# Kernel tuning notes

Measured on AMD Instinct MI355X. Metric: run time of the kernel, lower is better.

## Reference

```python
import jax, jax.numpy as jnp
import numpy as np

N_NODES = 50000
N_EDGES = 800000
D = 128            # input_dim == output_dim (no zero-padding branch in GatedGraphConv)
N_ETYPES = 4
N_STEPS = 8
B = 50
MAX_NODES = 1400
HID = 256


def setup_inputs() -> dict:
    key = jax.random.key(0)
    ks = jax.random.split(key, 10)
    # ragged graph sizes: alternating 600 / 1400 nodes, sums exactly to N_NODES
    counts = np.tile(np.array([600, 1400], dtype=np.int32), B // 2)
    s_d = 1.0 / np.sqrt(D)
    s_h = 1.0 / np.sqrt(HID)
    return {
        "node_features": jax.random.normal(ks[0], (N_NODES, D), jnp.float32),
        "edge_src": jax.random.randint(ks[1], (N_EDGES,), 0, N_NODES, dtype=jnp.int32),
        "edge_dst": jax.random.randint(ks[2], (N_EDGES,), 0, N_NODES, dtype=jnp.int32),
        "edge_types": jax.random.randint(ks[3], (N_EDGES,), 0, N_ETYPES, dtype=jnp.int32),
        "node_counts": jnp.asarray(counts),
        # per-edge-type message linears (DGL: one nn.Linear(out,out) per etype)
        "W_msg": jax.random.normal(ks[4], (N_ETYPES, D, D), jnp.float32) * s_d,
        "b_msg": jnp.zeros((N_ETYPES, D), jnp.float32),
        # GRUCell params (torch gate order: r, z, n)
        "W_ih": jax.random.normal(ks[5], (3 * D, D), jnp.float32) * s_d,
        "W_hh": jax.random.normal(ks[6], (3 * D, D), jnp.float32) * s_d,
        "b_ih": jnp.zeros((3 * D,), jnp.float32),
        "b_hh": jnp.zeros((3 * D,), jnp.float32),
        # classifier: Linear(D,256) + ReLU + Linear(256,1) + sigmoid (dropout = identity at eval)
        "W1": jax.random.normal(ks[7], (D, HID), jnp.float32) * s_d,
        "b1": jnp.zeros((HID,), jnp.float32),
        "W2": jax.random.normal(ks[8], (HID, 1), jnp.float32) * s_h,
        "b2": jnp.zeros((1,), jnp.float32),
    }


def _forward(node_features, edge_src, edge_dst, edge_types, node_counts,
             W_msg, b_msg, W_ih, W_hh, b_ih, b_hh, W1, b1, W2, b2):
    h = node_features
    for _ in range(N_STEPS):
        h_src = h[edge_src]                                   # [E, D] gather
        m = jnp.zeros_like(h_src)
        for t in range(N_ETYPES):                             # small fixed loop over edge types
            m = m + jnp.where((edge_types == t)[:, None],
                              h_src @ W_msg[t] + b_msg[t], 0.0)
        a = jax.ops.segment_sum(m, edge_dst, num_segments=N_NODES)  # [N, D] scatter-sum
        # GRUCell update
        gi = a @ W_ih.T + b_ih
        gh = h @ W_hh.T + b_hh
        i_r, i_z, i_n = jnp.split(gi, 3, axis=-1)
        h_r, h_z, h_n = jnp.split(gh, 3, axis=-1)
        r = jax.nn.sigmoid(i_r + h_r)
        z = jax.nn.sigmoid(i_z + h_z)
        n = jnp.tanh(i_n + r * h_n)
        h = (1.0 - z) * n + z * h
    # de-batchify to padded [B, MAX_NODES, D] + masked mean pool
    offsets = jnp.concatenate([jnp.zeros((1,), node_counts.dtype),
                               jnp.cumsum(node_counts)[:-1]])
    idx = offsets[:, None] + jnp.arange(MAX_NODES, dtype=node_counts.dtype)
    mask = jnp.arange(MAX_NODES)[None, :] < node_counts[:, None]
    g = h[jnp.clip(idx, 0, N_NODES - 1)] * mask[..., None]    # [B, MAX_NODES, D]
    pooled = g.sum(axis=1) / node_counts[:, None].astype(h.dtype)
    x = jax.nn.relu(pooled @ W1 + b1)
    return jax.nn.sigmoid(x @ W2 + b2)                        # [B, 1]


def reference(node_features, edge_src, edge_dst, edge_types, node_counts,
              W_msg, b_msg, W_ih, W_hh, b_ih, b_hh, W1, b1, W2, b2):
    return _forward(node_features, edge_src, edge_dst, edge_types, node_counts,
                    W_msg, b_msg, W_ih, W_hh, b_ih, b_hh, W1, b1, W2, b2)
```

## Files before the change

### kernel.cpp

```cpp
#include <hip/hip_runtime.h>
#include <hip/hip_bf16.h>

#define N_NODES 50000
#define N_EDGES 800000
#define D 128
#define N_ETYPES 4
#define N_STEPS 8
#define B_GRAPHS 50
#define HID 256
#define POOL_SPLIT 16
#define SCAN_B 196

typedef __attribute__((ext_vector_type(8))) short short8;
typedef __attribute__((ext_vector_type(4))) float f32x4;
typedef __attribute__((ext_vector_type(4))) unsigned uint4v;

static __device__ __forceinline__ unsigned short f2bf(float f) {
    union { float f; unsigned u; } v; v.f = f;
    unsigned r = v.u + 0x7FFF + ((v.u >> 16) & 1);
    return (unsigned short)(r >> 16);
}
static __device__ __forceinline__ float bf2f_u(unsigned s) {
    union { unsigned u; float f; } v; v.u = s << 16;
    return v.f;
}
static __device__ __forceinline__ float fsigmoid(float x) {
    return 1.f / (1.f + __expf(-x));
}
static __device__ __forceinline__ float ftanh(float x) {
    return 2.f / (1.f + __expf(-2.f * x)) - 1.f;
}

__global__ void k_init_h(const float* __restrict__ nf, unsigned short* __restrict__ hbf) {
    int i = blockIdx.x * blockDim.x + threadIdx.x;
    if (i < N_NODES * D) hbf[i] = f2bf(nf[i]);
}

__global__ void k_hist(const int* __restrict__ dst, int* __restrict__ deg) {
    int e = blockIdx.x * blockDim.x + threadIdx.x;
    if (e < N_EDGES) atomicAdd(&deg[dst[e]], 1);
}

__global__ __launch_bounds__(256) void k_scan1(const int* __restrict__ deg,
                                               int* __restrict__ bsum) {
    __shared__ int tmp[256];
    int t = threadIdx.x;
    int i = blockIdx.x * 256 + t;
    tmp[t] = (i < N_NODES) ? deg[i] : 0;
    __syncthreads();
    for (int s = 128; s > 0; s >>= 1) {
        if (t < s) tmp[t] += tmp[t + s];
        __syncthreads();
    }
    if (t == 0) bsum[blockIdx.x] = tmp[0];
}

__global__ __launch_bounds__(256) void k_scan2(const int* __restrict__ bsum,
                                               int* __restrict__ bpfx,
                                               int* __restrict__ rowptr) {
    __shared__ int part[256];
    int t = threadIdx.x;
    int v = (t < SCAN_B) ? bsum[t] : 0;
    part[t] = v;
    __syncthreads();
    for (int off = 1; off < 256; off <<= 1) {
        int u = (t >= off) ? part[t - off] : 0;
        __syncthreads();
        part[t] += u;
        __syncthreads();
    }
    if (t < SCAN_B) bpfx[t] = part[t] - v;
    if (t == SCAN_B - 1) rowptr[N_NODES] = part[t];
}

__global__ __launch_bounds__(256) void k_scan3(const int* __restrict__ deg,
                                               const int* __restrict__ bpfx,
                                               int* __restrict__ rowptr,
                                               int* __restrict__ cursor) {
    __shared__ int part[256];
    int t = threadIdx.x;
    int i = blockIdx.x * 256 + t;
    int v = (i < N_NODES) ? deg[i] : 0;
    part[t] = v;
    __syncthreads();
    for (int off = 1; off < 256; off <<= 1) {
        int u = (t >= off) ? part[t - off] : 0;
        __syncthreads();
        part[t] += u;
        __syncthreads();
    }
    if (i < N_NODES) {
        int rp = bpfx[blockIdx.x] + part[t] - v;
        rowptr[i] = rp;
        cursor[i] = rp;
    }
}

__global__ void k_fill(const int* __restrict__ src, const int* __restrict__ dst,
                       const int* __restrict__ et, int* __restrict__ cursor,
                       int* __restrict__ epack) {
    int e = blockIdx.x * blockDim.x + threadIdx.x;
    if (e < N_EDGES) {
        int slot = atomicAdd(&cursor[dst[e]], 1);
        epack[slot] = src[e] | (et[e] << 16);
    }
}

__global__ void k_pack(const float* __restrict__ Wmsg, const float* __restrict__ Wih,
                       const float* __restrict__ Whh, unsigned short* __restrict__ Pmsg,
                       unsigned short* __restrict__ Pih, unsigned short* __restrict__ Phh) {
    int bt = blockIdx.x;
    int l = threadIdx.x;
    if (bt < 128) {
        int nt = bt >> 4, kc = bt & 15;
        int n = nt * 16 + (l & 15);
        unsigned short* out = Pmsg + (((size_t)bt * 64 + l) * 8);
#pragma unroll
        for (int i = 0; i < 8; ++i) {
            int k = kc * 32 + ((l >> 4) << 3) + i;
            out[i] = f2bf(Wmsg[(size_t)(k >> 7) * (D * D) + (k & 127) * D + n]);
        }
        return;
    }
    const float* src;
    unsigned short* dstp;
    int id;
    if (bt < 224) { id = bt - 128; src = Wih; dstp = Pih; }
    else          { id = bt - 224; src = Whh; dstp = Phh; }
    int nt = id >> 2, c = id & 3;
    int n = nt * 16 + (l & 15);
    unsigned short* out = dstp + (((size_t)(nt * 4 + c) * 64 + l) * 8);
#pragma unroll
    for (int i = 0; i < 8; ++i) {
        int k = c * 32 + ((l >> 4) << 3) + i;
        out[i] = f2bf(src[n * D + k]);
    }
}

__global__ void k_pack_bias(const float* __restrict__ bih, const float* __restrict__ bhh,
                            float4* __restrict__ gb4) {
    int c = threadIdx.x;
    float4 g;
    g.x = bih[c] + bhh[c];
    g.y = bih[128 + c] + bhh[128 + c];
    g.z = bih[256 + c];
    g.w = bhh[256 + c];
    gb4[c] = g;
}

__global__ __launch_bounds__(256) void k_aggregate_s(const unsigned short* __restrict__ hbf,
                                                     const int* __restrict__ rowptr,
                                                     const int* __restrict__ epack,
                                                     unsigned short* __restrict__ S,
                                                     unsigned* __restrict__ deg4) {
    int w = threadIdx.x >> 6, l = threadIdx.x & 63;
    int v = blockIdx.x * 4 + w;
    if (v >= N_NODES) return;
    int lo = rowptr[v], hi = rowptr[v + 1];
    float a00 = 0.f, a01 = 0.f, a10 = 0.f, a11 = 0.f;
    float a20 = 0.f, a21 = 0.f, a30 = 0.f, a31 = 0.f;
    unsigned c0 = 0, c1 = 0, c2 = 0, c3 = 0;
    int i = lo;
    for (; i + 4 <= hi; i += 4) {
        int e0 = epack[i], e1 = epack[i + 1], e2 = epack[i + 2], e3 = epack[i + 3];
        unsigned x0 = *(const unsigned*)(hbf + ((size_t)(e0 & 0xFFFF) << 7) + 2 * l);
        unsigned x1 = *(const unsigned*)(hbf + ((size_t)(e1 & 0xFFFF) << 7) + 2 * l);
        unsigned x2 = *(const unsigned*)(hbf + ((size_t)(e2 & 0xFFFF) << 7) + 2 * l);
        unsigned x3 = *(const unsigned*)(hbf + ((size_t)(e3 & 0xFFFF) << 7) + 2 * l);
#define ACC_EDGE(e, x)                                                        \
        {                                                                     \
            int t_ = (e) >> 16;                                               \
            float lo_ = bf2f_u((x) & 0xFFFF), hi_ = bf2f_u((x) >> 16);        \
            if (t_ == 0)      { a00 += lo_; a01 += hi_; c0++; }               \
            else if (t_ == 1) { a10 += lo_; a11 += hi_; c1++; }               \
            else if (t_ == 2) { a20 += lo_; a21 += hi_; c2++; }               \
            else              { a30 += lo_; a31 += hi_; c3++; }               \
        }
        ACC_EDGE(e0, x0) ACC_EDGE(e1, x1) ACC_EDGE(e2, x2) ACC_EDGE(e3, x3)
    }
    for (; i < hi; ++i) {
        int e0 = epack[i];
        unsigned x0 = *(const unsigned*)(hbf + ((size_t)(e0 & 0xFFFF) << 7) + 2 * l);
        ACC_EDGE(e0, x0)
    }
#undef ACC_EDGE
    unsigned* Srow = (unsigned*)(S + (size_t)v * 512);
    Srow[l]       = (unsigned)f2bf(a00) | ((unsigned)f2bf(a01) << 16);
    Srow[64 + l]  = (unsigned)f2bf(a10) | ((unsigned)f2bf(a11) << 16);
    Srow[128 + l] = (unsigned)f2bf(a20) | ((unsigned)f2bf(a21) << 16);
    Srow[192 + l] = (unsigned)f2bf(a30) | ((unsigned)f2bf(a31) << 16);
    if (l == 0) {
        uint4v dg = {c0, c1, c2, c3};
        *(uint4v*)(deg4 + (size_t)v * 4) = dg;
    }
}

__global__ __launch_bounds__(256) void k_gemm_a(const unsigned short* __restrict__ S,
                                                const unsigned short* __restrict__ Pmsg,
                                                const unsigned* __restrict__ deg4,
                                                const float* __restrict__ bmsg,
                                                unsigned short* __restrict__ abf) {
    int tid = threadIdx.x, w = tid >> 6, l = tid & 63;
    int base = blockIdx.x * 64 + w * 16;
    int lr = l & 15, kb = l >> 4;
    int arow = base + lr; if (arow >= N_NODES) arow = N_NODES - 1;
    const short8* Sr = (const short8*)(S + (size_t)arow * 512);
    short8 af[16];
#pragma unroll
    for (int kc = 0; kc < 16; ++kc) af[kc] = Sr[kc * 4 + kb];
    uint4v dg[4];
#pragma unroll
    for (int j = 0; j < 4; ++j) {
        int row = base + kb * 4 + j; if (row >= N_NODES) row = N_NODES - 1;
        dg[j] = *(const uint4v*)(deg4 + (size_t)row * 4);
    }
    const short8* Bp = (const short8*)Pmsg;
#pragma unroll
    for (int ntp = 0; ntp < 4; ++ntp) {
        f32x4 acc0 = {0.f, 0.f, 0.f, 0.f}, acc1 = {0.f, 0.f, 0.f, 0.f};
#pragma unroll
        for (int kc = 0; kc < 16; ++kc) {
            short8 b0 = Bp[(((ntp * 2 + 0) * 16 + kc) * 64) + l];
            short8 b1 = Bp[(((ntp * 2 + 1) * 16 + kc) * 64) + l];
            acc0 = __builtin_amdgcn_mfma_f32_16x16x32_bf16(af[kc], b0, acc0, 0, 0, 0);
            acc1 = __builtin_amdgcn_mfma_f32_16x16x32_bf16(af[kc], b1, acc1, 0, 0, 0);
        }
#pragma unroll
        for (int half = 0; half < 2; ++half) {
            f32x4 acc = half ? acc1 : acc0;
            int col = (ntp * 2 + half) * 16 + lr;
            float b0 = bmsg[col], b1 = bmsg[128 + col], b2 = bmsg[256 + col], b3 = bmsg[384 + col];
#pragma unroll
            for (int j = 0; j < 4; ++j) {
                int row = base + kb * 4 + j;
                if (row < N_NODES) {
                    float bias = (float)dg[j].x * b0 + (float)dg[j].y * b1 +
                                 (float)dg[j].z * b2 + (float)dg[j].w * b3;
                    abf[(size_t)row * D + col] = f2bf(acc[j] + bias);
                }
            }
        }
    }
}

__global__ __launch_bounds__(256) void k_gru(const unsigned short* __restrict__ abf,
                                             unsigned short* __restrict__ hbf,
                                             const unsigned short* __restrict__ Pih,
                                             const unsigned short* __restrict__ Phh,
                                             const float4* __restrict__ gb4) {
    int tid = threadIdx.x, w = tid >> 6, l = tid & 63;
    int base = (blockIdx.x >> 1) * 64 + w * 16;
    int nt0 = (blockIdx.x & 1) * 4;
    int lr = l & 15, kb = l >> 4;
    int arow = base + lr; if (arow >= N_NODES) arow = N_NODES - 1;
    const short8* ar = (const short8*)(abf + (size_t)arow * D);
    const short8* hr = (const short8*)(hbf + (size_t)arow * D);
    short8 afa[4], afh[4];
#pragma unroll
    for (int c = 0; c < 4; ++c) { afa[c] = ar[c * 4 + kb]; afh[c] = hr[c * 4 + kb]; }
    const short8* Bi = (const short8*)Pih;
    const short8* Bh = (const short8*)Phh;
#pragma unroll
    for (int ntl = 0; ntl < 4; ++ntl) {
        int nt = nt0 + ntl;
        f32x4 racc = {0.f, 0.f, 0.f, 0.f};
        f32x4 zacc = {0.f, 0.f, 0.f, 0.f};
        f32x4 giacc = {0.f, 0.f, 0.f, 0.f};
        f32x4 ghacc = {0.f, 0.f, 0.f, 0.f};
#pragma unroll
        for (int c = 0; c < 4; ++c) {
            short8 bir = Bi[((0 * 8 + nt) * 4 + c) * 64 + l];
            short8 bhr = Bh[((0 * 8 + nt) * 4 + c) * 64 + l];
            short8 biz = Bi[((1 * 8 + nt) * 4 + c) * 64 + l];
            short8 bhz = Bh[((1 * 8 + nt) * 4 + c) * 64 + l];
            short8 bin = Bi[((2 * 8 + nt) * 4 + c) * 64 + l];
            short8 bhn = Bh[((2 * 8 + nt) * 4 + c) * 64 + l];
            racc = __builtin_amdgcn_mfma_f32_16x16x32_bf16(afa[c], bir, racc, 0, 0, 0);
            racc = __builtin_amdgcn_mfma_f32_16x16x32_bf16(afh[c], bhr, racc, 0, 0, 0);
            zacc = __builtin_amdgcn_mfma_f32_16x16x32_bf16(afa[c], biz, zacc, 0, 0, 0);
            zacc = __builtin_amdgcn_mfma_f32_16x16x32_bf16(afh[c], bhz, zacc, 0, 0, 0);
            giacc = __builtin_amdgcn_mfma_f32_16x16x32_bf16(afa[c], bin, giacc, 0, 0, 0);
            ghacc = __builtin_amdgcn_mfma_f32_16x16x32_bf16(afh[c], bhn, ghacc, 0, 0, 0);
        }
        int col = nt * 16 + lr;
        float4 gb = gb4[col];
#pragma unroll
        for (int j = 0; j < 4; ++j) {
            int row = base + kb * 4 + j;
            if (row < N_NODES) {
                float rr = fsigmoid(racc[j] + gb.x);
                float zz = fsigmoid(zacc[j] + gb.y);
                float nn = ftanh(giacc[j] + gb.z + rr * (ghacc[j] + gb.w));
                size_t idx = (size_t)row * D + col;
                float hold = bf2f_u(hbf[idx]);
                hbf[idx] = f2bf((1.f - zz) * nn + zz * hold);
            }
        }
    }
}

__global__ __launch_bounds__(256) void k_pool1(const unsigned short* __restrict__ hbf,
                                               const int* __restrict__ counts,
                                               float* __restrict__ partial) {
    __shared__ float tmp[256];
    int g = blockIdx.x / POOL_SPLIT;
    int j = blockIdx.x % POOL_SPLIT;
    int t = threadIdx.x;
    int offset = 0;
    for (int i = 0; i < g; ++i) offset += counts[i];
    int cnt = counts[g];
    int d = t & 127, half = t >> 7;
    float acc = 0.f;
    for (int r = 2 * j + half; r < cnt; r += 2 * POOL_SPLIT)
        acc += bf2f_u(hbf[(size_t)(offset + r) * D + d]);
    tmp[t] = acc;
    __syncthreads();
    if (t < D) partial[(size_t)(g * POOL_SPLIT + j) * D + t] = tmp[t] + tmp[t + 128];
}

__global__ __launch_bounds__(256) void k_pool2(const float* __restrict__ partial,
                                               const int* __restrict__ counts,
                                               const float* __restrict__ W1,
                                               const float* __restrict__ b1,
                                               const float* __restrict__ W2,
                                               const float* __restrict__ b2,
                                               float* __restrict__ out) {
    __shared__ float pooled[D];
    __shared__ float xh[HID];
    int g = blockIdx.x;
    int t = threadIdx.x;
    int cnt = counts[g];
    if (t < D) {
        float s = 0.f;
#pragma unroll
        for (int j = 0; j < POOL_SPLIT; ++j)
            s += partial[(size_t)(g * POOL_SPLIT + j) * D + t];
        pooled[t] = s / (float)cnt;
    }
    __syncthreads();
    float x = b1[t];
    for (int k = 0; k < D; ++k) x += pooled[k] * W1[k * HID + t];
    x = fmaxf(x, 0.f);
    xh[t] = x * W2[t];
    __syncthreads();
    for (int s = 128; s > 0; s >>= 1) {
        if (t < s) xh[t] += xh[t + s];
        __syncthreads();
    }
    if (t == 0) out[g] = 1.f / (1.f + __expf(-(xh[0] + b2[0])));
}

extern "C" void kernel_launch(void* const* d_in, const int* in_sizes, int n_in,
                              void* d_out, int out_size, void* d_ws, size_t ws_size,
                              hipStream_t stream) {
    const float* nf   = (const float*)d_in[0];
    const int* esrc   = (const int*)d_in[1];
    const int* edst   = (const int*)d_in[2];
    const int* etyp   = (const int*)d_in[3];
    const int* counts = (const int*)d_in[4];
    const float* Wmsg = (const float*)d_in[5];
    const float* bmsg = (const float*)d_in[6];
    const float* Wih  = (const float*)d_in[7];
    const float* Whh  = (const float*)d_in[8];
    const float* bih  = (const float*)d_in[9];
    const float* bhh  = (const float*)d_in[10];
    const float* W1   = (const float*)d_in[11];
    const float* b1   = (const float*)d_in[12];
    const float* W2   = (const float*)d_in[13];
    const float* b2   = (const float*)d_in[14];
    float* out = (float*)d_out;

    char* ws = (char*)d_ws;
    size_t off = 0;
    auto alloc = [&](size_t bytes) {
        void* p = ws + off;
        off = (off + bytes + 255) & ~(size_t)255;
        return p;
    };
    unsigned short* hbf = (unsigned short*)alloc((size_t)N_NODES * D * 2);
    unsigned short* abf = (unsigned short*)alloc((size_t)N_NODES * D * 2);
    unsigned short* S   = (unsigned short*)alloc((size_t)N_NODES * 512 * 2);
    unsigned short* Pmsg = (unsigned short*)alloc(128 * 64 * 8 * 2);
    unsigned short* Pih  = (unsigned short*)alloc(24 * 4 * 64 * 8 * 2);
    unsigned short* Phh  = (unsigned short*)alloc(24 * 4 * 64 * 8 * 2);
    float* gb4 = (float*)alloc(128 * 16);
    int* deg    = (int*)alloc((size_t)N_NODES * 4);
    unsigned* deg4 = (unsigned*)alloc((size_t)N_NODES * 16);
    int* rowptr = (int*)alloc((size_t)(N_NODES + 1) * 4);
    int* cursor = (int*)alloc((size_t)N_NODES * 4);
    int* epack  = (int*)alloc((size_t)N_EDGES * 4);
    float* partial = (float*)alloc((size_t)B_GRAPHS * POOL_SPLIT * D * 4);
    int* bsum = (int*)alloc(SCAN_B * 4);
    int* bpfx = (int*)alloc(SCAN_B * 4);

    hipMemsetAsync(deg, 0, (size_t)N_NODES * 4, stream);
    k_init_h<<<(N_NODES * D) / 256, 256, 0, stream>>>(nf, hbf);
    k_hist<<<N_EDGES / 256, 256, 0, stream>>>(edst, deg);
    k_scan1<<<SCAN_B, 256, 0, stream>>>(deg, bsum);
    k_scan2<<<1, 256, 0, stream>>>(bsum, bpfx, rowptr);
    k_scan3<<<SCAN_B, 256, 0, stream>>>(deg, bpfx, rowptr, cursor);
    k_fill<<<N_EDGES / 256, 256, 0, stream>>>(esrc, edst, etyp, cursor, epack);
    k_pack<<<320, 64, 0, stream>>>(Wmsg, Wih, Whh, Pmsg, Pih, Phh);
    k_pack_bias<<<1, 128, 0, stream>>>(bih, bhh, (float4*)gb4);

    int ga_blocks  = (N_NODES + 63) / 64;
    int gru_blocks = 2 * ((N_NODES + 63) / 64);
    int agg_blocks = (N_NODES + 3) / 4;
    for (int s = 0; s < N_STEPS; ++s) {
        k_aggregate_s<<<agg_blocks, 256, 0, stream>>>(hbf, rowptr, epack, S, deg4);
        k_gemm_a<<<ga_blocks, 256, 0, stream>>>(S, Pmsg, deg4, bmsg, abf);
        k_gru<<<gru_blocks, 256, 0, stream>>>(abf, hbf, Pih, Phh, (const float4*)gb4);
    }
    k_pool1<<<B_GRAPHS * POOL_SPLIT, 256, 0, stream>>>(hbf, counts, partial);
    k_pool2<<<B_GRAPHS, 256, 0, stream>>>(partial, counts, W1, b1, W2, b2, out);
}
```

Baseline: 1.065 ms.

## Fuse aggregation, message GEMM and GRU into one per-step kernel

Replaces the three per-step kernels (aggregate, message GEMM, GRU) with a single kernel. Each block handles 16 nodes and keeps the per-type sums and messages in swizzled shared memory instead of global S/abf buffers, with ping-pong h buffers so the in-place update stays race-free. This removes the global round-trips for S (1 KB per node) and abf, plus two launches per step. In exchange blocks are smaller (16 rows), each block re-reads all weight fragments, and the GEMM phases may run at lower occupancy because of the larger shared-memory footprint.

```diff
diff --git a/kernel.cpp b/kernel.cpp
--- a/kernel.cpp
+++ b/kernel.cpp
@@ -10,6 +10,7 @@
 #define HID 256
 #define POOL_SPLIT 16
 #define SCAN_B 196
+#define NPB 16
 
 typedef __attribute__((ext_vector_type(8))) short short8;
 typedef __attribute__((ext_vector_type(4))) float f32x4;
@@ -19,6 +20,9 @@
     union { float f; unsigned u; } v; v.f = f;
     unsigned r = v.u + 0x7FFF + ((v.u >> 16) & 1);
     return (unsigned short)(r >> 16);
+}
+static __device__ __forceinline__ unsigned pk2(float a, float b) {
+    return (unsigned)f2bf(a) | ((unsigned)f2bf(b) << 16);
 }
 static __device__ __forceinline__ float bf2f_u(unsigned s) {
     union { unsigned u; float f; } v; v.u = s << 16;
@@ -148,152 +152,146 @@
     gb4[c] = g;
 }
 
-__global__ __launch_bounds__(256) void k_aggregate_s(const unsigned short* __restrict__ hbf,
-                                                     const int* __restrict__ rowptr,
-                                                     const int* __restrict__ epack,
-                                                     unsigned short* __restrict__ S,
-                                                     unsigned* __restrict__ deg4) {
-    int w = threadIdx.x >> 6, l = threadIdx.x & 63;
-    int v = blockIdx.x * 4 + w;
-    if (v >= N_NODES) return;
-    int lo = rowptr[v], hi = rowptr[v + 1];
-    float a00 = 0.f, a01 = 0.f, a10 = 0.f, a11 = 0.f;
-    float a20 = 0.f, a21 = 0.f, a30 = 0.f, a31 = 0.f;
-    unsigned c0 = 0, c1 = 0, c2 = 0, c3 = 0;
-    int i = lo;
-    for (; i + 4 <= hi; i += 4) {
-        int e0 = epack[i], e1 = epack[i + 1], e2 = epack[i + 2], e3 = epack[i + 3];
-        unsigned x0 = *(const unsigned*)(hbf + ((size_t)(e0 & 0xFFFF) << 7) + 2 * l);
-        unsigned x1 = *(const unsigned*)(hbf + ((size_t)(e1 & 0xFFFF) << 7) + 2 * l);
-        unsigned x2 = *(const unsigned*)(hbf + ((size_t)(e2 & 0xFFFF) << 7) + 2 * l);
-        unsigned x3 = *(const unsigned*)(hbf + ((size_t)(e3 & 0xFFFF) << 7) + 2 * l);
+__global__ __launch_bounds__(256) void k_step(const unsigned short* __restrict__ hold,
+                                              unsigned short* __restrict__ hnew,
+                                              const int* __restrict__ rowptr,
+                                              const int* __restrict__ epack,
+                                              const unsigned short* __restrict__ Pmsg,
+                                              const unsigned short* __restrict__ Pih,
+                                              const unsigned short* __restrict__ Phh,
+                                              const float* __restrict__ bmsg,
+                                              const float4* __restrict__ gb4) {
+    __shared__ unsigned short Sh[NPB * 512];
+    __shared__ unsigned short Ah[NPB * 128];
+    __shared__ uint4v Dg[NPB];
+    int tid = threadIdx.x, w = tid >> 6, l = tid & 63;
+    int lr = l & 15, kb = l >> 4;
+    int nb = blockIdx.x * NPB;
+
+    for (int q = 0; q < 4; ++q) {
+        int n = w * 4 + q;
+        int v = nb + n;
+        int lo = rowptr[v], hi = rowptr[v + 1];
+        float a00 = 0.f, a01 = 0.f, a10 = 0.f, a11 = 0.f;
+        float a20 = 0.f, a21 = 0.f, a30 = 0.f, a31 = 0.f;
+        unsigned c0 = 0, c1 = 0, c2 = 0, c3 = 0;
+        int i = lo;
+        for (; i + 4 <= hi; i += 4) {
+            int e0 = epack[i], e1 = epack[i + 1], e2 = epack[i + 2], e3 = epack[i + 3];
+            unsigned x0 = *(const unsigned*)(hold + ((size_t)(e0 & 0xFFFF) << 7) + 2 * l);
+            unsigned x1 = *(const unsigned*)(hold + ((size_t)(e1 & 0xFFFF) << 7) + 2 * l);
+            unsigned x2 = *(const unsigned*)(hold + ((size_t)(e2 & 0xFFFF) << 7) + 2 * l);
+            unsigned x3 = *(const unsigned*)(hold + ((size_t)(e3 & 0xFFFF) << 7) + 2 * l);
 #define ACC_EDGE(e, x)                                                        \
-        {                                                                     \
-            int t_ = (e) >> 16;                                               \
-            float lo_ = bf2f_u((x) & 0xFFFF), hi_ = bf2f_u((x) >> 16);        \
-            if (t_ == 0)      { a00 += lo_; a01 += hi_; c0++; }               \
-            else if (t_ == 1) { a10 += lo_; a11 += hi_; c1++; }               \
-            else if (t_ == 2) { a20 += lo_; a21 += hi_; c2++; }               \
-            else              { a30 += lo_; a31 += hi_; c3++; }               \
-        }
-        ACC_EDGE(e0, x0) ACC_EDGE(e1, x1) ACC_EDGE(e2, x2) ACC_EDGE(e3, x3)
-    }
-    for (; i < hi; ++i) {
-        int e0 = epack[i];
-        unsigned x0 = *(const unsigned*)(hbf + ((size_t)(e0 & 0xFFFF) << 7) + 2 * l);
-        ACC_EDGE(e0, x0)
-    }
+            {                                                                 \
+                int t_ = (e) >> 16;                                           \
+                float lo_ = bf2f_u((x) & 0xFFFF), hi_ = bf2f_u((x) >> 16);    \
+                if (t_ == 0)      { a00 += lo_; a01 += hi_; c0++; }           \
+                else if (t_ == 1) { a10 += lo_; a11 += hi_; c1++; }           \
+                else if (t_ == 2) { a20 += lo_; a21 += hi_; c2++; }           \
+                else              { a30 += lo_; a31 += hi_; c3++; }           \
+            }
+            ACC_EDGE(e0, x0) ACC_EDGE(e1, x1) ACC_EDGE(e2, x2) ACC_EDGE(e3, x3)
+        }
+        for (; i < hi; ++i) {
+            int e0 = epack[i];
+            unsigned x0 = *(const unsigned*)(hold + ((size_t)(e0 & 0xFFFF) << 7) + 2 * l);
+            ACC_EDGE(e0, x0)
+        }
 #undef ACC_EDGE
-    unsigned* Srow = (unsigned*)(S + (size_t)v * 512);
-    Srow[l]       = (unsigned)f2bf(a00) | ((unsigned)f2bf(a01) << 16);
-    Srow[64 + l]  = (unsigned)f2bf(a10) | ((unsigned)f2bf(a11) << 16);
-    Srow[128 + l] = (unsigned)f2bf(a20) | ((unsigned)f2bf(a21) << 16);
-    Srow[192 + l] = (unsigned)f2bf(a30) | ((unsigned)f2bf(a31) << 16);
-    if (l == 0) {
-        uint4v dg = {c0, c1, c2, c3};
-        *(uint4v*)(deg4 + (size_t)v * 4) = dg;
-    }
-}
-
-__global__ __launch_bounds__(256) void k_gemm_a(const unsigned short* __restrict__ S,
-                                                const unsigned short* __restrict__ Pmsg,
-                                                const unsigned* __restrict__ deg4,
-                                                const float* __restrict__ bmsg,
-                                                unsigned short* __restrict__ abf) {
-    int tid = threadIdx.x, w = tid >> 6, l = tid & 63;
-    int base = blockIdx.x * 64 + w * 16;
-    int lr = l & 15, kb = l >> 4;
-    int arow = base + lr; if (arow >= N_NODES) arow = N_NODES - 1;
-    const short8* Sr = (const short8*)(S + (size_t)arow * 512);
-    short8 af[16];
-#pragma unroll
-    for (int kc = 0; kc < 16; ++kc) af[kc] = Sr[kc * 4 + kb];
-    uint4v dg[4];
-#pragma unroll
-    for (int j = 0; j < 4; ++j) {
-        int row = base + kb * 4 + j; if (row >= N_NODES) row = N_NODES - 1;
-        dg[j] = *(const uint4v*)(deg4 + (size_t)row * 4);
-    }
-    const short8* Bp = (const short8*)Pmsg;
-#pragma unroll
-    for (int ntp = 0; ntp < 4; ++ntp) {
+        unsigned swz = (unsigned)((n & 7) << 4);
+        char* rowp = (char*)Sh + n * 1024;
+        *(unsigned*)(rowp + ((4 * l) ^ swz))        = pk2(a00, a01);
+        *(unsigned*)(rowp + ((256 + 4 * l) ^ swz))  = pk2(a10, a11);
+        *(unsigned*)(rowp + ((512 + 4 * l) ^ swz))  = pk2(a20, a21);
+        *(unsigned*)(rowp + ((768 + 4 * l) ^ swz))  = pk2(a30, a31);
+        if (l == 0) { uint4v dgv = {c0, c1, c2, c3}; Dg[n] = dgv; }
+    }
+    __syncthreads();
+
+    {
         f32x4 acc0 = {0.f, 0.f, 0.f, 0.f}, acc1 = {0.f, 0.f, 0.f, 0.f};
+        const short8* Bp = (const short8*)Pmsg;
+        unsigned rswz = (unsigned)((lr & 7) << 4);
 #pragma unroll
         for (int kc = 0; kc < 16; ++kc) {
-            short8 b0 = Bp[(((ntp * 2 + 0) * 16 + kc) * 64) + l];
-            short8 b1 = Bp[(((ntp * 2 + 1) * 16 + kc) * 64) + l];
-            acc0 = __builtin_amdgcn_mfma_f32_16x16x32_bf16(af[kc], b0, acc0, 0, 0, 0);
-            acc1 = __builtin_amdgcn_mfma_f32_16x16x32_bf16(af[kc], b1, acc1, 0, 0, 0);
-        }
-#pragma unroll
-        for (int half = 0; half < 2; ++half) {
-            f32x4 acc = half ? acc1 : acc0;
-            int col = (ntp * 2 + half) * 16 + lr;
+            short8 af = *(const short8*)((const char*)Sh + lr * 1024 +
+                                         (((unsigned)(kc * 64 + kb * 16)) ^ rswz));
+            short8 b0 = Bp[(size_t)(w * 16 + kc) * 64 + l];
+            short8 b1 = Bp[(size_t)((w + 4) * 16 + kc) * 64 + l];
+            acc0 = __builtin_amdgcn_mfma_f32_16x16x32_bf16(af, b0, acc0, 0, 0, 0);
+            acc1 = __builtin_amdgcn_mfma_f32_16x16x32_bf16(af, b1, acc1, 0, 0, 0);
+        }
+#pragma unroll
+        for (int t = 0; t < 2; ++t) {
+            int nt = w + t * 4;
+            int col = nt * 16 + lr;
             float b0 = bmsg[col], b1 = bmsg[128 + col], b2 = bmsg[256 + col], b3 = bmsg[384 + col];
+            f32x4 acc = t ? acc1 : acc0;
 #pragma unroll
             for (int j = 0; j < 4; ++j) {
-                int row = base + kb * 4 + j;
-                if (row < N_NODES) {
-                    float bias = (float)dg[j].x * b0 + (float)dg[j].y * b1 +
-                                 (float)dg[j].z * b2 + (float)dg[j].w * b3;
-                    abf[(size_t)row * D + col] = f2bf(acc[j] + bias);
-                }
+                int row = kb * 4 + j;
+                uint4v dgv = Dg[row];
+                float av = acc[j] + (float)dgv.x * b0 + (float)dgv.y * b1 +
+                           (float)dgv.z * b2 + (float)dgv.w * b3;
+                *(unsigned short*)((char*)Ah + row * 256 +
+                                   (((unsigned)(2 * col)) ^ ((unsigned)((row & 7) << 4)))) = f2bf(av);
             }
         }
     }
-}
-
-__global__ __launch_bounds__(256) void k_gru(const unsigned short* __restrict__ abf,
-                                             unsigned short* __restrict__ hbf,
-                                             const unsigned short* __restrict__ Pih,
-                                             const unsigned short* __restrict__ Phh,
-                                             const float4* __restrict__ gb4) {
-    int tid = threadIdx.x, w = tid >> 6, l = tid & 63;
-    int base = (blockIdx.x >> 1) * 64 + w * 16;
-    int nt0 = (blockIdx.x & 1) * 4;
-    int lr = l & 15, kb = l >> 4;
-    int arow = base + lr; if (arow >= N_NODES) arow = N_NODES - 1;
-    const short8* ar = (const short8*)(abf + (size_t)arow * D);
-    const short8* hr = (const short8*)(hbf + (size_t)arow * D);
-    short8 afa[4], afh[4];
-#pragma unroll
-    for (int c = 0; c < 4; ++c) { afa[c] = ar[c * 4 + kb]; afh[c] = hr[c * 4 + kb]; }
-    const short8* Bi = (const short8*)Pih;
-    const short8* Bh = (const short8*)Phh;
-#pragma unroll
-    for (int ntl = 0; ntl < 4; ++ntl) {
-        int nt = nt0 + ntl;
-        f32x4 racc = {0.f, 0.f, 0.f, 0.f};
-        f32x4 zacc = {0.f, 0.f, 0.f, 0.f};
-        f32x4 giacc = {0.f, 0.f, 0.f, 0.f};
-        f32x4 ghacc = {0.f, 0.f, 0.f, 0.f};
+    __syncthreads();
+
+    {
+        const short8* hrow = (const short8*)(hold + (size_t)(nb + lr) * D);
+        short8 afh[4];
+#pragma unroll
+        for (int c = 0; c < 4; ++c) afh[c] = hrow[c * 4 + kb];
+        f32x4 racc[2], zacc[2], giacc[2], ghacc[2];
+#pragma unroll
+        for (int t = 0; t < 2; ++t) {
+            racc[t] = (f32x4){0.f, 0.f, 0.f, 0.f};
+            zacc[t] = (f32x4){0.f, 0.f, 0.f, 0.f};
+            giacc[t] = (f32x4){0.f, 0.f, 0.f, 0.f};
+            ghacc[t] = (f32x4){0.f, 0.f, 0.f, 0.f};
+        }
+        const short8* Bi = (const short8*)Pih;
+        const short8* Bh = (const short8*)Phh;
+        unsigned rswz = (unsigned)((lr & 7) << 4);
 #pragma unroll
         for (int c = 0; c < 4; ++c) {
-            short8 bir = Bi[((0 * 8 + nt) * 4 + c) * 64 + l];
-            short8 bhr = Bh[((0 * 8 + nt) * 4 + c) * 64 + l];
-            short8 biz = Bi[((1 * 8 + nt) * 4 + c) * 64 + l];
-            short8 bhz = Bh[((1 * 8 + nt) * 4 + c) * 64 + l];
-            short8 bin = Bi[((2 * 8 + nt) * 4 + c) * 64 + l];
-            short8 bhn = Bh[((2 * 8 + nt) * 4 + c) * 64 + l];
-            racc = __builtin_amdgcn_mfma_f32_16x16x32_bf16(afa[c], bir, racc, 0, 0, 0);
-            racc = __builtin_amdgcn_mfma_f32_16x16x32_bf16(afh[c], bhr, racc, 0, 0, 0);
-            zacc = __builtin_amdgcn_mfma_f32_16x16x32_bf16(afa[c], biz, zacc, 0, 0, 0);
-            zacc = __builtin_amdgcn_mfma_f32_16x16x32_bf16(afh[c], bhz, zacc, 0, 0, 0);
-            giacc = __builtin_amdgcn_mfma_f32_16x16x32_bf16(afa[c], bin, giacc, 0, 0, 0);
-            ghacc = __builtin_amdgcn_mfma_f32_16x16x32_bf16(afh[c], bhn, ghacc, 0, 0, 0);
-        }
-        int col = nt * 16 + lr;
-        float4 gb = gb4[col];
-#pragma unroll
-        for (int j = 0; j < 4; ++j) {
-            int row = base + kb * 4 + j;
-            if (row < N_NODES) {
-                float rr = fsigmoid(racc[j] + gb.x);
-                float zz = fsigmoid(zacc[j] + gb.y);
-                float nn = ftanh(giacc[j] + gb.z + rr * (ghacc[j] + gb.w));
+            short8 afa = *(const short8*)((const char*)Ah + lr * 256 +
+                                          (((unsigned)(c * 64 + kb * 16)) ^ rswz));
+#pragma unroll
+            for (int t = 0; t < 2; ++t) {
+                int nt = w + t * 4;
+                short8 bir = Bi[(size_t)((0 + nt) * 4 + c) * 64 + l];
+                short8 bhr = Bh[(size_t)((0 + nt) * 4 + c) * 64 + l];
+                short8 biz = Bi[(size_t)((8 + nt) * 4 + c) * 64 + l];
+                short8 bhz = Bh[(size_t)((8 + nt) * 4 + c) * 64 + l];
+                short8 bin = Bi[(size_t)((16 + nt) * 4 + c) * 64 + l];
+                short8 bhn = Bh[(size_t)((16 + nt) * 4 + c) * 64 + l];
+                racc[t] = __builtin_amdgcn_mfma_f32_16x16x32_bf16(afa, bir, racc[t], 0, 0, 0);
+                racc[t] = __builtin_amdgcn_mfma_f32_16x16x32_bf16(afh[c], bhr, racc[t], 0, 0, 0);
+                zacc[t] = __builtin_amdgcn_mfma_f32_16x16x32_bf16(afa, biz, zacc[t], 0, 0, 0);
+                zacc[t] = __builtin_amdgcn_mfma_f32_16x16x32_bf16(afh[c], bhz, zacc[t], 0, 0, 0);
+                giacc[t] = __builtin_amdgcn_mfma_f32_16x16x32_bf16(afa, bin, giacc[t], 0, 0, 0);
+                ghacc[t] = __builtin_amdgcn_mfma_f32_16x16x32_bf16(afh[c], bhn, ghacc[t], 0, 0, 0);
+            }
+        }
+#pragma unroll
+        for (int t = 0; t < 2; ++t) {
+            int nt = w + t * 4;
+            int col = nt * 16 + lr;
+            float4 gb = gb4[col];
+#pragma unroll
+            for (int j = 0; j < 4; ++j) {
+                int row = nb + kb * 4 + j;
+                float rr = fsigmoid(racc[t][j] + gb.x);
+                float zz = fsigmoid(zacc[t][j] + gb.y);
+                float nn = ftanh(giacc[t][j] + gb.z + rr * (ghacc[t][j] + gb.w));
                 size_t idx = (size_t)row * D + col;
-                float hold = bf2f_u(hbf[idx]);
-                hbf[idx] = f2bf((1.f - zz) * nn + zz * hold);
+                float hv = bf2f_u(hold[idx]);
+                hnew[idx] = f2bf((1.f - zz) * nn + zz * hv);
             }
         }
     }
@@ -377,15 +375,13 @@
         off = (off + bytes + 255) & ~(size_t)255;
         return p;
     };
-    unsigned short* hbf = (unsigned short*)alloc((size_t)N_NODES * D * 2);
-    unsigned short* abf = (unsigned short*)alloc((size_t)N_NODES * D * 2);
-    unsigned short* S   = (unsigned short*)alloc((size_t)N_NODES * 512 * 2);
+    unsigned short* hbf0 = (unsigned short*)alloc((size_t)N_NODES * D * 2);
+    unsigned short* hbf1 = (unsigned short*)alloc((size_t)N_NODES * D * 2);
     unsigned short* Pmsg = (unsigned short*)alloc(128 * 64 * 8 * 2);
     unsigned short* Pih  = (unsigned short*)alloc(24 * 4 * 64 * 8 * 2);
     unsigned short* Phh  = (unsigned short*)alloc(24 * 4 * 64 * 8 * 2);
     float* gb4 = (float*)alloc(128 * 16);
     int* deg    = (int*)alloc((size_t)N_NODES * 4);
-    unsigned* deg4 = (unsigned*)alloc((size_t)N_NODES * 16);
     int* rowptr = (int*)alloc((size_t)(N_NODES + 1) * 4);
     int* cursor = (int*)alloc((size_t)N_NODES * 4);
     int* epack  = (int*)alloc((size_t)N_EDGES * 4);
@@ -394,7 +390,7 @@
     int* bpfx = (int*)alloc(SCAN_B * 4);
 
     hipMemsetAsync(deg, 0, (size_t)N_NODES * 4, stream);
-    k_init_h<<<(N_NODES * D) / 256, 256, 0, stream>>>(nf, hbf);
+    k_init_h<<<(N_NODES * D) / 256, 256, 0, stream>>>(nf, hbf0);
     k_hist<<<N_EDGES / 256, 256, 0, stream>>>(edst, deg);
     k_scan1<<<SCAN_B, 256, 0, stream>>>(deg, bsum);
     k_scan2<<<1, 256, 0, stream>>>(bsum, bpfx, rowptr);
@@ -403,14 +399,14 @@
     k_pack<<<320, 64, 0, stream>>>(Wmsg, Wih, Whh, Pmsg, Pih, Phh);
     k_pack_bias<<<1, 128, 0, stream>>>(bih, bhh, (float4*)gb4);
 
-    int ga_blocks  = (N_NODES + 63) / 64;
-    int gru_blocks = 2 * ((N_NODES + 63) / 64);
-    int agg_blocks = (N_NODES + 3) / 4;
+    const int step_blocks = N_NODES / NPB;
     for (int s = 0; s < N_STEPS; ++s) {
-        k_aggregate_s<<<agg_blocks, 256, 0, stream>>>(hbf, rowptr, epack, S, deg4);
-        k_gemm_a<<<ga_blocks, 256, 0, stream>>>(S, Pmsg, deg4, bmsg, abf);
-        k_gru<<<gru_blocks, 256, 0, stream>>>(abf, hbf, Pih, Phh, (const float4*)gb4);
-    }
-    k_pool1<<<B_GRAPHS * POOL_SPLIT, 256, 0, stream>>>(hbf, counts, partial);
+        const unsigned short* hold = (s & 1) ? hbf1 : hbf0;
+        unsigned short* hnew       = (s & 1) ? hbf0 : hbf1;
+        k_step<<<step_blocks, 256, 0, stream>>>(hold, hnew, rowptr, epack,
+                                                Pmsg, Pih, Phh, bmsg,
+                                                (const float4*)gb4);
+    }
+    k_pool1<<<B_GRAPHS * POOL_SPLIT, 256, 0, stream>>>(hbf0, counts, partial);
     k_pool2<<<B_GRAPHS, 256, 0, stream>>>(partial, counts, W1, b1, W2, b2, out);
 }
```

New measurement: 1.113 ms. 4.5% more time.

## Bucket CSR by (node, edge type) to remove per-edge type branching

Applied to the files above, without the earlier changes.

Builds the CSR keyed by node*4+etype, so each node's edges are pre-sorted by type. The aggregate kernel can then sum each type segment with branch-free code, using pre-shifted byte offsets, and derive degrees from rowptr instead of writing deg4. The message GEMM is split across twice as many blocks, and h is double-buffered between steps. This costs a larger scan over 200k entries and extra rowptr reads, and the inner loops for short per-type segments become shorter.

```diff
diff --git a/kernel.cpp b/kernel.cpp
--- a/kernel.cpp
+++ b/kernel.cpp
@@ -9,21 +9,34 @@
 #define B_GRAPHS 50
 #define HID 256
 #define POOL_SPLIT 16
-#define SCAN_B 196
+#define N4 (N_NODES * N_ETYPES)
+#define SCAN_B4 ((N4 + 255) / 256)
 
 typedef __attribute__((ext_vector_type(8))) short short8;
 typedef __attribute__((ext_vector_type(4))) float f32x4;
 typedef __attribute__((ext_vector_type(4))) unsigned uint4v;
+typedef __attribute__((ext_vector_type(4))) int int4v;
 
 static __device__ __forceinline__ unsigned short f2bf(float f) {
     union { float f; unsigned u; } v; v.f = f;
     unsigned r = v.u + 0x7FFF + ((v.u >> 16) & 1);
     return (unsigned short)(r >> 16);
 }
+static __device__ __forceinline__ unsigned pk2(float a, float b) {
+    return (unsigned)f2bf(a) | ((unsigned)f2bf(b) << 16);
+}
 static __device__ __forceinline__ float bf2f_u(unsigned s) {
     union { unsigned u; float f; } v; v.u = s << 16;
     return v.f;
 }
+static __device__ __forceinline__ float bflo(unsigned x) {
+    union { unsigned u; float f; } v; v.u = x << 16;
+    return v.f;
+}
+static __device__ __forceinline__ float bfhi(unsigned x) {
+    union { unsigned u; float f; } v; v.u = x & 0xFFFF0000u;
+    return v.f;
+}
 static __device__ __forceinline__ float fsigmoid(float x) {
     return 1.f / (1.f + __expf(-x));
 }
@@ -36,17 +49,18 @@
     if (i < N_NODES * D) hbf[i] = f2bf(nf[i]);
 }
 
-__global__ void k_hist(const int* __restrict__ dst, int* __restrict__ deg) {
+__global__ void k_hist(const int* __restrict__ dst, const int* __restrict__ et,
+                       int* __restrict__ deg4) {
     int e = blockIdx.x * blockDim.x + threadIdx.x;
-    if (e < N_EDGES) atomicAdd(&deg[dst[e]], 1);
-}
-
-__global__ __launch_bounds__(256) void k_scan1(const int* __restrict__ deg,
+    if (e < N_EDGES) atomicAdd(&deg4[dst[e] * 4 + et[e]], 1);
+}
+
+__global__ __launch_bounds__(256) void k_scan1(const int* __restrict__ deg4,
                                                int* __restrict__ bsum) {
     __shared__ int tmp[256];
     int t = threadIdx.x;
     int i = blockIdx.x * 256 + t;
-    tmp[t] = (i < N_NODES) ? deg[i] : 0;
+    tmp[t] = (i < N4) ? deg4[i] : 0;
     __syncthreads();
     for (int s = 128; s > 0; s >>= 1) {
         if (t < s) tmp[t] += tmp[t + s];
@@ -55,32 +69,32 @@
     if (t == 0) bsum[blockIdx.x] = tmp[0];
 }
 
-__global__ __launch_bounds__(256) void k_scan2(const int* __restrict__ bsum,
-                                               int* __restrict__ bpfx,
-                                               int* __restrict__ rowptr) {
-    __shared__ int part[256];
+__global__ __launch_bounds__(1024) void k_scan2(const int* __restrict__ bsum,
+                                                int* __restrict__ bpfx,
+                                                int* __restrict__ rowptr4) {
+    __shared__ int part[1024];
     int t = threadIdx.x;
-    int v = (t < SCAN_B) ? bsum[t] : 0;
+    int v = (t < SCAN_B4) ? bsum[t] : 0;
     part[t] = v;
     __syncthreads();
-    for (int off = 1; off < 256; off <<= 1) {
+    for (int off = 1; off < 1024; off <<= 1) {
         int u = (t >= off) ? part[t - off] : 0;
         __syncthreads();
         part[t] += u;
         __syncthreads();
     }
-    if (t < SCAN_B) bpfx[t] = part[t] - v;
-    if (t == SCAN_B - 1) rowptr[N_NODES] = part[t];
-}
-
-__global__ __launch_bounds__(256) void k_scan3(const int* __restrict__ deg,
+    if (t < SCAN_B4) bpfx[t] = part[t] - v;
+    if (t == SCAN_B4 - 1) rowptr4[N4] = part[t];
+}
+
+__global__ __launch_bounds__(256) void k_scan3(const int* __restrict__ deg4,
                                                const int* __restrict__ bpfx,
-                                               int* __restrict__ rowptr,
-                                               int* __restrict__ cursor) {
+                                               int* __restrict__ rowptr4,
+                                               int* __restrict__ cursor4) {
     __shared__ int part[256];
     int t = threadIdx.x;
     int i = blockIdx.x * 256 + t;
-    int v = (i < N_NODES) ? deg[i] : 0;
+    int v = (i < N4) ? deg4[i] : 0;
     part[t] = v;
     __syncthreads();
     for (int off = 1; off < 256; off <<= 1) {
@@ -89,20 +103,20 @@
         part[t] += u;
         __syncthreads();
     }
-    if (i < N_NODES) {
+    if (i < N4) {
         int rp = bpfx[blockIdx.x] + part[t] - v;
-        rowptr[i] = rp;
-        cursor[i] = rp;
+        rowptr4[i] = rp;
+        cursor4[i] = rp;
     }
 }
 
 __global__ void k_fill(const int* __restrict__ src, const int* __restrict__ dst,
-                       const int* __restrict__ et, int* __restrict__ cursor,
+                       const int* __restrict__ et, int* __restrict__ cursor4,
                        int* __restrict__ epack) {
     int e = blockIdx.x * blockDim.x + threadIdx.x;
     if (e < N_EDGES) {
-        int slot = atomicAdd(&cursor[dst[e]], 1);
-        epack[slot] = src[e] | (et[e] << 16);
+        int slot = atomicAdd(&cursor4[dst[e] * 4 + et[e]], 1);
+        epack[slot] = src[e] << 8;
     }
 }
 
@@ -148,94 +162,95 @@
     gb4[c] = g;
 }
 
-__global__ __launch_bounds__(256) void k_aggregate_s(const unsigned short* __restrict__ hbf,
-                                                     const int* __restrict__ rowptr,
+__global__ __launch_bounds__(256) void k_aggregate_s(const unsigned short* __restrict__ hold,
+                                                     const int* __restrict__ rowptr4,
                                                      const int* __restrict__ epack,
-                                                     unsigned short* __restrict__ S,
-                                                     unsigned* __restrict__ deg4) {
+                                                     unsigned short* __restrict__ S) {
     int w = threadIdx.x >> 6, l = threadIdx.x & 63;
     int v = blockIdx.x * 4 + w;
     if (v >= N_NODES) return;
-    int lo = rowptr[v], hi = rowptr[v + 1];
-    float a00 = 0.f, a01 = 0.f, a10 = 0.f, a11 = 0.f;
-    float a20 = 0.f, a21 = 0.f, a30 = 0.f, a31 = 0.f;
-    unsigned c0 = 0, c1 = 0, c2 = 0, c3 = 0;
-    int i = lo;
-    for (; i + 4 <= hi; i += 4) {
-        int e0 = epack[i], e1 = epack[i + 1], e2 = epack[i + 2], e3 = epack[i + 3];
-        unsigned x0 = *(const unsigned*)(hbf + ((size_t)(e0 & 0xFFFF) << 7) + 2 * l);
-        unsigned x1 = *(const unsigned*)(hbf + ((size_t)(e1 & 0xFFFF) << 7) + 2 * l);
-        unsigned x2 = *(const unsigned*)(hbf + ((size_t)(e2 & 0xFFFF) << 7) + 2 * l);
-        unsigned x3 = *(const unsigned*)(hbf + ((size_t)(e3 & 0xFFFF) << 7) + 2 * l);
-#define ACC_EDGE(e, x)                                                        \
-        {                                                                     \
-            int t_ = (e) >> 16;                                               \
-            float lo_ = bf2f_u((x) & 0xFFFF), hi_ = bf2f_u((x) >> 16);        \
-            if (t_ == 0)      { a00 += lo_; a01 += hi_; c0++; }               \
-            else if (t_ == 1) { a10 += lo_; a11 += hi_; c1++; }               \
-            else if (t_ == 2) { a20 += lo_; a21 += hi_; c2++; }               \
-            else              { a30 += lo_; a31 += hi_; c3++; }               \
-        }
-        ACC_EDGE(e0, x0) ACC_EDGE(e1, x1) ACC_EDGE(e2, x2) ACC_EDGE(e3, x3)
-    }
-    for (; i < hi; ++i) {
-        int e0 = epack[i];
-        unsigned x0 = *(const unsigned*)(hbf + ((size_t)(e0 & 0xFFFF) << 7) + 2 * l);
-        ACC_EDGE(e0, x0)
-    }
-#undef ACC_EDGE
+    int4v b = *(const int4v*)(rowptr4 + v * 4);
+    int b4 = rowptr4[v * 4 + 4];
+    const char* hp = (const char*)hold + 4 * l;
     unsigned* Srow = (unsigned*)(S + (size_t)v * 512);
-    Srow[l]       = (unsigned)f2bf(a00) | ((unsigned)f2bf(a01) << 16);
-    Srow[64 + l]  = (unsigned)f2bf(a10) | ((unsigned)f2bf(a11) << 16);
-    Srow[128 + l] = (unsigned)f2bf(a20) | ((unsigned)f2bf(a21) << 16);
-    Srow[192 + l] = (unsigned)f2bf(a30) | ((unsigned)f2bf(a31) << 16);
-    if (l == 0) {
-        uint4v dg = {c0, c1, c2, c3};
-        *(uint4v*)(deg4 + (size_t)v * 4) = dg;
+#pragma unroll
+    for (int t = 0; t < 4; ++t) {
+        int i  = (t == 0) ? b.x : (t == 1) ? b.y : (t == 2) ? b.z : b.w;
+        int hi = (t == 0) ? b.y : (t == 1) ? b.z : (t == 2) ? b.w : b4;
+        float a0 = 0.f, a1 = 0.f;
+        for (; i + 4 <= hi; i += 4) {
+            int s0 = epack[i], s1 = epack[i + 1], s2 = epack[i + 2], s3 = epack[i + 3];
+            unsigned x0 = *(const unsigned*)(hp + s0);
+            unsigned x1 = *(const unsigned*)(hp + s1);
+            unsigned x2 = *(const unsigned*)(hp + s2);
+            unsigned x3 = *(const unsigned*)(hp + s3);
+            a0 += bflo(x0) + bflo(x1) + bflo(x2) + bflo(x3);
+            a1 += bfhi(x0) + bfhi(x1) + bfhi(x2) + bfhi(x3);
+        }
+        if (i + 2 <= hi) {
+            int s0 = epack[i], s1 = epack[i + 1];
+            unsigned x0 = *(const unsigned*)(hp + s0);
+            unsigned x1 = *(const unsigned*)(hp + s1);
+            a0 += bflo(x0) + bflo(x1);
+            a1 += bfhi(x0) + bfhi(x1);
+            i += 2;
+        }
+        if (i < hi) {
+            unsigned x0 = *(const unsigned*)(hp + epack[i]);
+            a0 += bflo(x0);
+            a1 += bfhi(x0);
+        }
+        Srow[t * 64 + l] = pk2(a0, a1);
     }
 }
 
 __global__ __launch_bounds__(256) void k_gemm_a(const unsigned short* __restrict__ S,
                                                 const unsigned short* __restrict__ Pmsg,
-                                                const unsigned* __restrict__ deg4,
+                                                const int* __restrict__ rowptr4,
                                                 const float* __restrict__ bmsg,
                                                 unsigned short* __restrict__ abf) {
     int tid = threadIdx.x, w = tid >> 6, l = tid & 63;
-    int base = blockIdx.x * 64 + w * 16;
+    int base = (blockIdx.x >> 1) * 64 + w * 16;
+    int nh = (blockIdx.x & 1) * 4;
     int lr = l & 15, kb = l >> 4;
     int arow = base + lr; if (arow >= N_NODES) arow = N_NODES - 1;
     const short8* Sr = (const short8*)(S + (size_t)arow * 512);
     short8 af[16];
 #pragma unroll
     for (int kc = 0; kc < 16; ++kc) af[kc] = Sr[kc * 4 + kb];
-    uint4v dg[4];
+    float dgf[4][4];
 #pragma unroll
     for (int j = 0; j < 4; ++j) {
         int row = base + kb * 4 + j; if (row >= N_NODES) row = N_NODES - 1;
-        dg[j] = *(const uint4v*)(deg4 + (size_t)row * 4);
+        int4v r4 = *(const int4v*)(rowptr4 + row * 4);
+        int r5 = rowptr4[row * 4 + 4];
+        dgf[j][0] = (float)(r4.y - r4.x);
+        dgf[j][1] = (float)(r4.z - r4.y);
+        dgf[j][2] = (float)(r4.w - r4.z);
+        dgf[j][3] = (float)(r5 - r4.w);
     }
     const short8* Bp = (const short8*)Pmsg;
 #pragma unroll
-    for (int ntp = 0; ntp < 4; ++ntp) {
+    for (int ntp = 0; ntp < 2; ++ntp) {
+        int nt0 = nh + ntp * 2;
         f32x4 acc0 = {0.f, 0.f, 0.f, 0.f}, acc1 = {0.f, 0.f, 0.f, 0.f};
 #pragma unroll
         for (int kc = 0; kc < 16; ++kc) {
-            short8 b0 = Bp[(((ntp * 2 + 0) * 16 + kc) * 64) + l];
-            short8 b1 = Bp[(((ntp * 2 + 1) * 16 + kc) * 64) + l];
+            short8 b0 = Bp[(size_t)((nt0 + 0) * 16 + kc) * 64 + l];
+            short8 b1 = Bp[(size_t)((nt0 + 1) * 16 + kc) * 64 + l];
             acc0 = __builtin_amdgcn_mfma_f32_16x16x32_bf16(af[kc], b0, acc0, 0, 0, 0);
             acc1 = __builtin_amdgcn_mfma_f32_16x16x32_bf16(af[kc], b1, acc1, 0, 0, 0);
         }
 #pragma unroll
         for (int half = 0; half < 2; ++half) {
             f32x4 acc = half ? acc1 : acc0;
-            int col = (ntp * 2 + half) * 16 + lr;
+            int col = (nt0 + half) * 16 + lr;
             float b0 = bmsg[col], b1 = bmsg[128 + col], b2 = bmsg[256 + col], b3 = bmsg[384 + col];
 #pragma unroll
             for (int j = 0; j < 4; ++j) {
                 int row = base + kb * 4 + j;
                 if (row < N_NODES) {
-                    float bias = (float)dg[j].x * b0 + (float)dg[j].y * b1 +
-                                 (float)dg[j].z * b2 + (float)dg[j].w * b3;
+                    float bias = dgf[j][0] * b0 + dgf[j][1] * b1 + dgf[j][2] * b2 + dgf[j][3] * b3;
                     abf[(size_t)row * D + col] = f2bf(acc[j] + bias);
                 }
             }
@@ -244,7 +259,8 @@
 }
 
 __global__ __launch_bounds__(256) void k_gru(const unsigned short* __restrict__ abf,
-                                             unsigned short* __restrict__ hbf,
+                                             const unsigned short* __restrict__ hold,
+                                             unsigned short* __restrict__ hnew,
                                              const unsigned short* __restrict__ Pih,
                                              const unsigned short* __restrict__ Phh,
                                              const float4* __restrict__ gb4) {
@@ -254,7 +270,7 @@
     int lr = l & 15, kb = l >> 4;
     int arow = base + lr; if (arow >= N_NODES) arow = N_NODES - 1;
     const short8* ar = (const short8*)(abf + (size_t)arow * D);
-    const short8* hr = (const short8*)(hbf + (size_t)arow * D);
+    const short8* hr = (const short8*)(hold + (size_t)arow * D);
     short8 afa[4], afh[4];
 #pragma unroll
     for (int c = 0; c < 4; ++c) { afa[c] = ar[c * 4 + kb]; afh[c] = hr[c * 4 + kb]; }
@@ -292,8 +308,8 @@
                 float zz = fsigmoid(zacc[j] + gb.y);
                 float nn = ftanh(giacc[j] + gb.z + rr * (ghacc[j] + gb.w));
                 size_t idx = (size_t)row * D + col;
-                float hold = bf2f_u(hbf[idx]);
-                hbf[idx] = f2bf((1.f - zz) * nn + zz * hold);
+                float hv = bf2f_u(hold[idx]);
+                hnew[idx] = f2bf((1.f - zz) * nn + zz * hv);
             }
         }
     }
@@ -377,40 +393,43 @@
         off = (off + bytes + 255) & ~(size_t)255;
         return p;
     };
-    unsigned short* hbf = (unsigned short*)alloc((size_t)N_NODES * D * 2);
-    unsigned short* abf = (unsigned short*)alloc((size_t)N_NODES * D * 2);
-    unsigned short* S   = (unsigned short*)alloc((size_t)N_NODES * 512 * 2);
+    unsigned short* hbf0 = (unsigned short*)alloc((size_t)N_NODES * D * 2);
+    unsigned short* hbf1 = (unsigned short*)alloc((size_t)N_NODES * D * 2);
+    unsigned short* abf  = (unsigned short*)alloc((size_t)N_NODES * D * 2);
+    unsigned short* S    = (unsigned short*)alloc((size_t)N_NODES * 512 * 2);
     unsigned short* Pmsg = (unsigned short*)alloc(128 * 64 * 8 * 2);
     unsigned short* Pih  = (unsigned short*)alloc(24 * 4 * 64 * 8 * 2);
     unsigned short* Phh  = (unsigned short*)alloc(24 * 4 * 64 * 8 * 2);
     float* gb4 = (float*)alloc(128 * 16);
-    int* deg    = (int*)alloc((size_t)N_NODES * 4);
-    unsigned* deg4 = (unsigned*)alloc((size_t)N_NODES * 16);
-    int* rowptr = (int*)alloc((size_t)(N_NODES + 1) * 4);
-    int* cursor = (int*)alloc((size_t)N_NODES * 4);
-    int* epack  = (int*)alloc((size_t)N_EDGES * 4);
+    int* deg4    = (int*)alloc((size_t)N4 * 4);
+    int* rowptr4 = (int*)alloc((size_t)(N4 + 1) * 4);
+    int* cursor4 = (int*)alloc((size_t)N4 * 4);
+    int* epack   = (int*)alloc((size_t)N_EDGES * 4);
     float* partial = (float*)alloc((size_t)B_GRAPHS * POOL_SPLIT * D * 4);
-    int* bsum = (int*)alloc(SCAN_B * 4);
-    int* bpfx = (int*)alloc(SCAN_B * 4);
-
-    hipMemsetAsync(deg, 0, (size_t)N_NODES * 4, stream);
-    k_init_h<<<(N_NODES * D) / 256, 256, 0, stream>>>(nf, hbf);
-    k_hist<<<N_EDGES / 256, 256, 0, stream>>>(edst, deg);
-    k_scan1<<<SCAN_B, 256, 0, stream>>>(deg, bsum);
-    k_scan2<<<1, 256, 0, stream>>>(bsum, bpfx, rowptr);
-    k_scan3<<<SCAN_B, 256, 0, stream>>>(deg, bpfx, rowptr, cursor);
-    k_fill<<<N_EDGES / 256, 256, 0, stream>>>(esrc, edst, etyp, cursor, epack);
+    int* bsum = (int*)alloc(SCAN_B4 * 4);
+    int* bpfx = (int*)alloc(SCAN_B4 * 4);
+
+    hipMemsetAsync(deg4, 0, (size_t)N4 * 4, stream);
+    k_init_h<<<(N_NODES * D) / 256, 256, 0, stream>>>(nf, hbf0);
+    k_hist<<<N_EDGES / 256, 256, 0, stream>>>(edst, etyp, deg4);
+    k_scan1<<<SCAN_B4, 256, 0, stream>>>(deg4, bsum);
+    k_scan2<<<1, 1024, 0, stream>>>(bsum, bpfx, rowptr4);
+    k_scan3<<<SCAN_B4, 256, 0, stream>>>(deg4, bpfx, rowptr4, cursor4);
+    k_fill<<<N_EDGES / 256, 256, 0, stream>>>(esrc, edst, etyp, cursor4, epack);
     k_pack<<<320, 64, 0, stream>>>(Wmsg, Wih, Whh, Pmsg, Pih, Phh);
     k_pack_bias<<<1, 128, 0, stream>>>(bih, bhh, (float4*)gb4);
 
-    int ga_blocks  = (N_NODES + 63) / 64;
+    int ga_blocks  = 2 * ((N_NODES + 63) / 64);
     int gru_blocks = 2 * ((N_NODES + 63) / 64);
     int agg_blocks = (N_NODES + 3) / 4;
     for (int s = 0; s < N_STEPS; ++s) {
-        k_aggregate_s<<<agg_blocks, 256, 0, stream>>>(hbf, rowptr, epack, S, deg4);
-        k_gemm_a<<<ga_blocks, 256, 0, stream>>>(S, Pmsg, deg4, bmsg, abf);
-        k_gru<<<gru_blocks, 256, 0, stream>>>(abf, hbf, Pih, Phh, (const float4*)gb4);
-    }
-    k_pool1<<<B_GRAPHS * POOL_SPLIT, 256, 0, stream>>>(hbf, counts, partial);
+        const unsigned short* hold = (s & 1) ? hbf1 : hbf0;
+        unsigned short* hnew       = (s & 1) ? hbf0 : hbf1;
+        k_aggregate_s<<<agg_blocks, 256, 0, stream>>>(hold, rowptr4, epack, S);
+        k_gemm_a<<<ga_blocks, 256, 0, stream>>>(S, Pmsg, rowptr4, bmsg, abf);
+        k_gru<<<gru_blocks, 256, 0, stream>>>(abf, hold, hnew, Pih, Phh,
+                                              (const float4*)gb4);
+    }
+    k_pool1<<<B_GRAPHS * POOL_SPLIT, 256, 0, stream>>>(hbf0, counts, partial);
     k_pool2<<<B_GRAPHS, 256, 0, stream>>>(partial, counts, W1, b1, W2, b2, out);
 }
```

New measurement: 1.054 ms. About the same (-1.0%).
